# Kernel optimization log

Measured on AMD Instinct MI355X. Metric: run time of the kernel, lower is better.

## Reference

```python
import jax, jax.numpy as jnp
import numpy as np

ZMAX = 92          # max atomic number in NLH table
BOHR = 0.52917721  # Bohr radius in Angstrom (au.BOHR)
ENERGY_UNIT = 1.0  # multiplier for 'Ha'
N_ATOMS = 100_000
N_EDGES = 6_400_000
TAB = (ZMAX + 1) ** 2  # 8649


def setup_inputs() -> dict:
    key = jax.random.key(0)
    k1, k2, k3, k4, k5, k6, k7 = jax.random.split(key, 7)
    species = jax.random.randint(k1, (N_ATOMS,), 0, 93, dtype=jnp.int32)
    edge_src = jax.random.randint(k2, (N_EDGES,), 0, N_ATOMS, dtype=jnp.int32)
    edge_dst = jax.random.randint(k3, (N_EDGES,), 0, N_ATOMS, dtype=jnp.int32)
    # distances kept away from zero (division by rijs)
    distances = 0.5 + 4.5 * jax.random.uniform(k4, (N_EDGES,), dtype=jnp.float32)
    switch = jax.random.uniform(k5, (N_EDGES,), dtype=jnp.float32)
    CS = jax.random.uniform(k6, (TAB, 3), dtype=jnp.float32)
    ALPHAS = jax.random.uniform(k7, (TAB, 3), dtype=jnp.float32) + 0.5
    return {"species": species, "edge_src": edge_src, "edge_dst": edge_dst,
            "distances": distances, "switch": switch, "CS": CS, "ALPHAS": ALPHAS}


def reference(species, edge_src, edge_dst, distances, switch, CS, ALPHAS):
    # pair index into (zmax+1)^2 coefficient table
    s12 = species[edge_src] + ZMAX * species[edge_dst]
    cs = CS[s12]          # [E, 3]
    alphas = ALPHAS[s12]  # [E, 3]
    Z = jnp.where(species > 0, species.astype(distances.dtype), 0.0)
    # 3-term exponential screening function
    phi = jnp.sum(cs * jnp.exp(-alphas * distances[:, None]), axis=-1)  # [E]
    ereppair = Z[edge_src] * Z[edge_dst] * phi * switch / distances
    erep_atomic = ENERGY_UNIT * 0.5 * BOHR * jax.ops.segment_sum(
        ereppair, edge_src, num_segments=species.shape[0])
    return erep_atomic
```

## Files before the change

kernel.cpp:

```cpp
#include <hip/hip_runtime.h>
#include <hip/hip_fp16.h>


#define ZMAX_C 92
#define TAB93  93
#define NTAB   (TAB93 * TAB93)
#define HALF_BOHR 0.264588605f
#define NBMAX 64
#define APB 2048
#define APB_LOG 11
#define SPLITS 16
#define TPB  1024
#define NW   (TPB / 64)
#define TPB2 256
#define EPT 8
#define BLK_EDGES (TPB * EPT)
#define SPC_CAP 122880

typedef int            ivec4 __attribute__((ext_vector_type(4)));
typedef float          fvec4 __attribute__((ext_vector_type(4)));

#if __has_builtin(__builtin_amdgcn_rcpf)
#define FAST_RCP(x) __builtin_amdgcn_rcpf(x)
#else
#define FAST_RCP(x) (1.0f / (x))
#endif

__device__ __forceinline__ float half_lo(unsigned u) {
    return __half2float(*reinterpret_cast<const __half*>(&u));
}
__device__ __forceinline__ float half_hi(unsigned u) {
    unsigned s = u >> 16;
    return __half2float(*reinterpret_cast<const __half*>(&s));
}

__global__ __launch_bounds__(TPB2) void p0_prep(
    const float* __restrict__ CS, const float* __restrict__ ALPHAS,
    const int* __restrict__ species,
    uint4* __restrict__ tab16, unsigned char* __restrict__ spc8,
    unsigned* __restrict__ cursor, float* __restrict__ out,
    int n_atoms, int nb)
{
    int i = blockIdx.x * TPB2 + threadIdx.x;
    if (i < NTAB) {
        int sd = i / TAB93;
        int ss = i - TAB93 * sd;
        int ref = ss + ZMAX_C * sd;
        float Z = (ss > 0 && sd > 0) ? (float)(ss * sd) : 0.0f;
        __half h[8];
        h[0] = __float2half_rn(CS[3*ref+0] * Z);
        h[1] = __float2half_rn(CS[3*ref+1] * Z);
        h[2] = __float2half_rn(CS[3*ref+2] * Z);
        h[3] = __float2half_rn(-ALPHAS[3*ref+0]);
        h[4] = __float2half_rn(-ALPHAS[3*ref+1]);
        h[5] = __float2half_rn(-ALPHAS[3*ref+2]);
        h[6] = __half(0.0f); h[7] = __half(0.0f);
        tab16[i] = *reinterpret_cast<uint4*>(h);
    }
    if (i < n_atoms) {
        spc8[i] = (unsigned char)species[i];
        out[i] = 0.0f;
    }
    if (i < nb) cursor[i] = 0u;
}

__global__ __launch_bounds__(TPB) void p1_bin_lds(
    const int* __restrict__ edge_src, const int* __restrict__ edge_dst,
    const float* __restrict__ dist, const float* __restrict__ swt,
    const unsigned char* __restrict__ spc8, const uint4* __restrict__ tab16,
    unsigned* __restrict__ pairs, unsigned* __restrict__ cursor,
    int nb, int cap, int n_edges, int n_atoms, int nchunks)
{
    __shared__ unsigned char spcL[SPC_CAP];
    __shared__ unsigned stage[BLK_EDGES];
    __shared__ unsigned histW[NW][NBMAX];
    __shared__ unsigned hist[NBMAX];
    __shared__ unsigned lbase[NBMAX];
    __shared__ unsigned gbase[NBMAX];

    int tid = threadIdx.x, bid = blockIdx.x;
    const int G = gridDim.x;
    int lane = tid & 63, wave = tid >> 6;

    {
        uint4* dv = (uint4*)spcL;
        const uint4* sv = (const uint4*)spc8;
        int n16 = (n_atoms + 15) >> 4;
        for (int i = tid; i < n16; i += TPB) dv[i] = sv[i];
    }
    __syncthreads();

    for (int c = bid; c < nchunks; c += G) {
        ((unsigned*)histW)[tid] = 0u;
        __syncthreads();

        long long wbase = (long long)c * BLK_EDGES + (long long)wave * (64 * EPT);
        unsigned meta[EPT];
        unsigned short s12r[EPT];

        {
            int srcv[EPT], dstv[EPT];
            #pragma unroll
            for (int j = 0; j < EPT / 4; ++j) {
                long long e0 = wbase + j * 256 + lane * 4;
                if (e0 + 3 < (long long)n_edges) {
                    ivec4 s4 = *reinterpret_cast<const ivec4*>(edge_src + e0);
                    ivec4 d4 = *reinterpret_cast<const ivec4*>(edge_dst + e0);
                    #pragma unroll
                    for (int k = 0; k < 4; ++k) { srcv[j*4+k] = s4[k]; dstv[j*4+k] = d4[k]; }
                } else {
                    #pragma unroll
                    for (int k = 0; k < 4; ++k) {
                        long long e = e0 + k;
                        bool v = (e < (long long)n_edges);
                        srcv[j*4+k] = v ? edge_src[e] : 0;
                        dstv[j*4+k] = v ? edge_dst[e] : 0;
                    }
                }
            }
            int ssv[EPT], sdv[EPT];
            #pragma unroll
            for (int i = 0; i < EPT; ++i) ssv[i] = spcL[srcv[i]];
            #pragma unroll
            for (int i = 0; i < EPT; ++i) sdv[i] = spcL[dstv[i]];
            #pragma unroll
            for (int j = 0; j < EPT / 4; ++j) {
                long long e0 = wbase + j * 256 + lane * 4;
                #pragma unroll
                for (int k = 0; k < 4; ++k) {
                    int idx = j * 4 + k;
                    s12r[idx] = (unsigned short)(ssv[idx] + TAB93 * sdv[idx]);
                    meta[idx] = 0u;
                    if (e0 + k < (long long)n_edges) {
                        unsigned b    = (unsigned)srcv[idx] >> APB_LOG;
                        unsigned lsrc = (unsigned)srcv[idx] & (APB - 1);
                        unsigned rank = atomicAdd(&histW[wave][b], 1u);
                        meta[idx] = 0x80000000u | (rank << 17) | (b << 11) | lsrc;
                    }
                }
            }
        }
        __syncthreads();
        if (tid < 64) {
            unsigned run = 0;
            #pragma unroll
            for (int w = 0; w < NW; ++w) {
                unsigned t = histW[w][tid];
                histW[w][tid] = run;
                run += t;
            }
            unsigned tot = run;
            if (tid < nb) hist[tid] = tot;
            unsigned v = (tid < nb) ? tot : 0u;
            unsigned x = v;
            #pragma unroll
            for (int off = 1; off < 64; off <<= 1) {
                unsigned y = __shfl_up(x, off);
                if ((tid & 63) >= off) x += y;
            }
            if (tid < nb) {
                lbase[tid] = x - v;
                gbase[tid] = v ? atomicAdd(cursor + tid, v) : 0u;
            }
        }
        __syncthreads();

        {
            long long eA = wbase + lane * 4;
            long long eB = wbase + 256 + lane * 4;
            float rA[4], wA[4], rB[4], wB[4];
            bool fullB = (eB + 3 < (long long)n_edges);
            if (fullB) {
                fvec4 r4 = *reinterpret_cast<const fvec4*>(dist + eA);
                fvec4 w4 = *reinterpret_cast<const fvec4*>(swt + eA);
                fvec4 r5 = *reinterpret_cast<const fvec4*>(dist + eB);
                fvec4 w5 = *reinterpret_cast<const fvec4*>(swt + eB);
                #pragma unroll
                for (int k = 0; k < 4; ++k) {
                    rA[k] = r4[k]; wA[k] = w4[k]; rB[k] = r5[k]; wB[k] = w5[k];
                }
            } else {
                #pragma unroll
                for (int k = 0; k < 4; ++k) {
                    long long ea = eA + k, eb = eB + k;
                    bool va = (ea < (long long)n_edges), vb = (eb < (long long)n_edges);
                    rA[k] = va ? dist[ea] : 1.f;  wA[k] = va ? swt[ea] : 0.f;
                    rB[k] = vb ? dist[eb] : 1.f;  wB[k] = vb ? swt[eb] : 0.f;
                }
            }
            uint4 tA[4], tB[4];
            #pragma unroll
            for (int k = 0; k < 4; ++k) tA[k] = tab16[s12r[k]];
            #pragma unroll
            for (int k = 0; k < 4; ++k) tB[k] = tab16[s12r[4 + k]];
            #pragma unroll
            for (int g = 0; g < 2; ++g) {
                const float* r = g ? rB : rA;
                const float* w = g ? wB : wA;
                const uint4* t = g ? tB : tA;
                #pragma unroll
                for (int k = 0; k < 4; ++k) {
                    int idx = g * 4 + k;
                    unsigned m = meta[idx];
                    if (!(m & 0x80000000u)) continue;
                    float c0 = half_lo(t[k].x), c1 = half_hi(t[k].x);
                    float c2 = half_lo(t[k].y), na0 = half_hi(t[k].y);
                    float na1 = half_lo(t[k].z), na2 = half_hi(t[k].z);
                    float phi = c0 * __expf(na0 * r[k])
                              + c1 * __expf(na1 * r[k])
                              + c2 * __expf(na2 * r[k]);
                    float val = HALF_BOHR * phi * w[k] * FAST_RCP(r[k]);
                    unsigned b = (m >> 11) & 63u;
                    unsigned pos = lbase[b] + histW[wave][b] + ((m >> 17) & 0x3FFFu);
                    unsigned short hb = __half_as_ushort(__float2half_rn(val));
                    stage[pos] = ((m & (APB - 1)) << 16) | (unsigned)hb;
                }
            }
        }
        __syncthreads();
        for (int b = wave; b < nb; b += NW) {
            unsigned cnt = hist[b], lb = lbase[b], gb = gbase[b];
            unsigned* dst = pairs + (size_t)b * (size_t)cap + gb;
            for (unsigned i = lane; i < cnt; i += 64)
                if (gb + i < (unsigned)cap) dst[i] = stage[lb + i];
        }
    }
}

#define TPBF 256
#define NWF  4
#define BLKF (TPBF * EPT)
__global__ __launch_bounds__(TPBF) void p1_bin(
    const int* __restrict__ edge_src, const int* __restrict__ edge_dst,
    const float* __restrict__ dist, const float* __restrict__ swt,
    const unsigned char* __restrict__ spc8, const uint4* __restrict__ tab16,
    unsigned* __restrict__ pairs, unsigned* __restrict__ cursor,
    int nb, int cap, int n_edges)
{
    __shared__ unsigned stage[BLKF];
    __shared__ unsigned hist4[NWF][NBMAX];
    __shared__ unsigned hist[NBMAX];
    __shared__ unsigned lbase[NBMAX];
    __shared__ unsigned gbase[NBMAX];

    int tid = threadIdx.x;
    ((unsigned*)hist4)[tid] = 0u;
    __syncthreads();

    int lane = tid & 63, wave = tid >> 6;
    long long wbase = (long long)blockIdx.x * BLKF + (long long)wave * (64 * EPT);

    unsigned meta[EPT];
    unsigned short s12r[EPT];
    {
        int srcv[EPT], dstv[EPT];
        #pragma unroll
        for (int j = 0; j < EPT / 4; ++j) {
            long long e0 = wbase + j * 256 + lane * 4;
            if (e0 + 3 < (long long)n_edges) {
                ivec4 s4 = *reinterpret_cast<const ivec4*>(edge_src + e0);
                ivec4 d4 = *reinterpret_cast<const ivec4*>(edge_dst + e0);
                #pragma unroll
                for (int k = 0; k < 4; ++k) { srcv[j*4+k] = s4[k]; dstv[j*4+k] = d4[k]; }
            } else {
                #pragma unroll
                for (int k = 0; k < 4; ++k) {
                    long long e = e0 + k;
                    bool v = (e < (long long)n_edges);
                    srcv[j*4+k] = v ? edge_src[e] : 0;
                    dstv[j*4+k] = v ? edge_dst[e] : 0;
                }
            }
        }
        int ssv[EPT], sdv[EPT];
        #pragma unroll
        for (int i = 0; i < EPT; ++i) ssv[i] = spc8[srcv[i]];
        #pragma unroll
        for (int i = 0; i < EPT; ++i) sdv[i] = spc8[dstv[i]];
        #pragma unroll
        for (int j = 0; j < EPT / 4; ++j) {
            long long e0 = wbase + j * 256 + lane * 4;
            #pragma unroll
            for (int k = 0; k < 4; ++k) {
                int idx = j * 4 + k;
                s12r[idx] = (unsigned short)(ssv[idx] + TAB93 * sdv[idx]);
                meta[idx] = 0u;
                if (e0 + k < (long long)n_edges) {
                    unsigned b    = (unsigned)srcv[idx] >> APB_LOG;
                    unsigned lsrc = (unsigned)srcv[idx] & (APB - 1);
                    unsigned rank = atomicAdd(&hist4[wave][b], 1u);
                    meta[idx] = 0x80000000u | (rank << 17) | (b << 11) | lsrc;
                }
            }
        }
    }
    __syncthreads();
    if (tid < 64) {
        unsigned run = 0;
        #pragma unroll
        for (int w = 0; w < NWF; ++w) {
            unsigned t = hist4[w][tid];
            hist4[w][tid] = run;
            run += t;
        }
        unsigned tot = run;
        if (tid < nb) hist[tid] = tot;
        unsigned v = (tid < nb) ? tot : 0u;
        unsigned x = v;
        #pragma unroll
        for (int off = 1; off < 64; off <<= 1) {
            unsigned y = __shfl_up(x, off);
            if ((tid & 63) >= off) x += y;
        }
        if (tid < nb) {
            lbase[tid] = x - v;
            gbase[tid] = v ? atomicAdd(cursor + tid, v) : 0u;
        }
    }
    __syncthreads();
    {
        long long eA = wbase + lane * 4;
        long long eB = wbase + 256 + lane * 4;
        float rA[4], wA[4], rB[4], wB[4];
        bool fullB = (eB + 3 < (long long)n_edges);
        if (fullB) {
            fvec4 r4 = *reinterpret_cast<const fvec4*>(dist + eA);
            fvec4 w4 = *reinterpret_cast<const fvec4*>(swt + eA);
            fvec4 r5 = *reinterpret_cast<const fvec4*>(dist + eB);
            fvec4 w5 = *reinterpret_cast<const fvec4*>(swt + eB);
            #pragma unroll
            for (int k = 0; k < 4; ++k) {
                rA[k] = r4[k]; wA[k] = w4[k]; rB[k] = r5[k]; wB[k] = w5[k];
            }
        } else {
            #pragma unroll
            for (int k = 0; k < 4; ++k) {
                long long ea = eA + k, eb = eB + k;
                bool va = (ea < (long long)n_edges), vb = (eb < (long long)n_edges);
                rA[k] = va ? dist[ea] : 1.f;  wA[k] = va ? swt[ea] : 0.f;
                rB[k] = vb ? dist[eb] : 1.f;  wB[k] = vb ? swt[eb] : 0.f;
            }
        }
        uint4 tA[4], tB[4];
        #pragma unroll
        for (int k = 0; k < 4; ++k) tA[k] = tab16[s12r[k]];
        #pragma unroll
        for (int k = 0; k < 4; ++k) tB[k] = tab16[s12r[4 + k]];
        #pragma unroll
        for (int g = 0; g < 2; ++g) {
            const float* r = g ? rB : rA;
            const float* w = g ? wB : wA;
            const uint4* t = g ? tB : tA;
            #pragma unroll
            for (int k = 0; k < 4; ++k) {
                int idx = g * 4 + k;
                unsigned m = meta[idx];
                if (!(m & 0x80000000u)) continue;
                float c0 = half_lo(t[k].x), c1 = half_hi(t[k].x);
                float c2 = half_lo(t[k].y), na0 = half_hi(t[k].y);
                float na1 = half_lo(t[k].z), na2 = half_hi(t[k].z);
                float phi = c0 * __expf(na0 * r[k])
                          + c1 * __expf(na1 * r[k])
                          + c2 * __expf(na2 * r[k]);
                float val = HALF_BOHR * phi * w[k] * FAST_RCP(r[k]);
                unsigned b = (m >> 11) & 63u;
                unsigned pos = lbase[b] + hist4[wave][b] + ((m >> 17) & 0x3FFFu);
                unsigned short hb = __half_as_ushort(__float2half_rn(val));
                stage[pos] = ((m & (APB - 1)) << 16) | (unsigned)hb;
            }
        }
    }
    __syncthreads();
    for (int b = wave; b < nb; b += NWF) {
        unsigned cnt = hist[b], lb = lbase[b], gb = gbase[b];
        unsigned* dst = pairs + (size_t)b * (size_t)cap + gb;
        for (unsigned i = lane; i < cnt; i += 64)
            if (gb + i < (unsigned)cap) dst[i] = stage[lb + i];
    }
}

__global__ __launch_bounds__(TPB2) void p2a_reduce(
    const unsigned* __restrict__ pairs, const unsigned* __restrict__ cursor,
    float* __restrict__ out, int cap, int n_atoms)
{
    int b = blockIdx.x / SPLITS;
    int s = blockIdx.x % SPLITS;
    __shared__ float acc[APB];
    for (int i = threadIdx.x; i < APB; i += TPB2) acc[i] = 0.f;
    __syncthreads();
    unsigned cnt = cursor[b];
    if (cnt > (unsigned)cap) cnt = (unsigned)cap;
    unsigned nq = (cnt + 3u) >> 2;
    unsigned qb = (unsigned)((unsigned long long)nq * s / SPLITS);
    unsigned qe = (unsigned)((unsigned long long)nq * (s + 1) / SPLITS);
    const uint4* p4 = (const uint4*)(pairs + (size_t)b * (size_t)cap);
    for (unsigned q = qb + threadIdx.x; q < qe; q += TPB2) {
        uint4 v = p4[q];
        unsigned base = q << 2;
        if (base + 3u < cnt) {
            unsafeAtomicAdd(&acc[v.x >> 16], __half2float(__ushort_as_half((unsigned short)(v.x & 0xFFFFu))));
            unsafeAtomicAdd(&acc[v.y >> 16], __half2float(__ushort_as_half((unsigned short)(v.y & 0xFFFFu))));
            unsafeAtomicAdd(&acc[v.z >> 16], __half2float(__ushort_as_half((unsigned short)(v.z & 0xFFFFu))));
            unsafeAtomicAdd(&acc[v.w >> 16], __half2float(__ushort_as_half((unsigned short)(v.w & 0xFFFFu))));
        } else {
            unsigned vv[4] = {v.x, v.y, v.z, v.w};
            #pragma unroll
            for (int e = 0; e < 4; ++e)
                if (base + (unsigned)e < cnt)
                    unsafeAtomicAdd(&acc[vv[e] >> 16],
                        __half2float(__ushort_as_half((unsigned short)(vv[e] & 0xFFFFu))));
        }
    }
    __syncthreads();
    int abase = b * APB;
    for (int k = threadIdx.x; k < APB; k += TPB2) {
        int atom = abase + k;
        float vv = acc[k];
        if (atom < n_atoms && vv != 0.0f)
            unsafeAtomicAdd(&out[atom], vv);
    }
}

__global__ __launch_bounds__(TPB2) void erep_edges_direct(
    const int* __restrict__ edge_src, const int* __restrict__ edge_dst,
    const float* __restrict__ dist, const float* __restrict__ swt,
    const int* __restrict__ species, const float* __restrict__ CS,
    const float* __restrict__ ALPHAS, float* __restrict__ out, int n_edges)
{
    int e = blockIdx.x * TPB2 + threadIdx.x;
    if (e >= n_edges) return;
    int ss = species[edge_src[e]], sd = species[edge_dst[e]];
    int prod = ss * sd;
    if (prod == 0) return;
    int s12 = ss + ZMAX_C * sd;
    float r = dist[e];
    float phi = CS[3*s12+0] * __expf(-ALPHAS[3*s12+0] * r)
              + CS[3*s12+1] * __expf(-ALPHAS[3*s12+1] * r)
              + CS[3*s12+2] * __expf(-ALPHAS[3*s12+2] * r);
    atomicAdd(out + edge_src[e],
              HALF_BOHR * (float)prod * phi * swt[e] * FAST_RCP(r));
}

extern "C" void kernel_launch(void* const* d_in, const int* in_sizes, int n_in,
                              void* d_out, int out_size, void* d_ws, size_t ws_size,
                              hipStream_t stream)
{
    const int*   species  = (const int*)  d_in[0];
    const int*   edge_src = (const int*)  d_in[1];
    const int*   edge_dst = (const int*)  d_in[2];
    const float* dist     = (const float*)d_in[3];
    const float* swt      = (const float*)d_in[4];
    const float* CS       = (const float*)d_in[5];
    const float* ALPHAS   = (const float*)d_in[6];
    float* out = (float*)d_out;

    int n_atoms = in_sizes[0];
    int n_edges = in_sizes[1];

    int nb = (n_atoms + APB - 1) / APB;
    long long capll = (long long)n_edges / nb + (long long)n_edges / ((long long)nb * 32) + 256;
    int cap = (int)((capll + 31) & ~31LL);

    size_t pairs_sz = ((size_t)nb * (size_t)cap * 4 + 255) & ~(size_t)255;
    size_t cur_sz   = ((size_t)nb * 4 + 255) & ~(size_t)255;
    size_t tab_sz   = ((size_t)NTAB * 16 + 255) & ~(size_t)255;
    size_t spc_sz   = ((size_t)n_atoms + 255) & ~(size_t)255;
    size_t need = pairs_sz + cur_sz + tab_sz + spc_sz;

    if (nb <= NBMAX && n_edges > 0 && ws_size >= need) {
        char* w = (char*)d_ws;
        unsigned*       pairs   = (unsigned*)w;
        unsigned*       cursor  = (unsigned*)(w + pairs_sz);
        uint4*          tab16   = (uint4*)(w + pairs_sz + cur_sz);
        unsigned char*  spc8    = (unsigned char*)(w + pairs_sz + cur_sz + tab_sz);

        int pmax = n_atoms > NTAB ? n_atoms : NTAB;
        p0_prep<<<(pmax + TPB2 - 1) / TPB2, TPB2, 0, stream>>>(
            CS, ALPHAS, species, tab16, spc8, cursor, out, n_atoms, nb);

        if (n_atoms <= SPC_CAP) {
            int dev = 0, ncu = 256;
            (void)hipGetDevice(&dev);
            (void)hipDeviceGetAttribute(&ncu, hipDeviceAttributeMultiprocessorCount, dev);
            int nchunks = (int)(((long long)n_edges + BLK_EDGES - 1) / BLK_EDGES);
            int G = ncu > 0 ? ncu : 256;
            if (G > nchunks) G = nchunks;
            p1_bin_lds<<<G, TPB, 0, stream>>>(
                edge_src, edge_dst, dist, swt, spc8, tab16,
                pairs, cursor, nb, cap, n_edges, n_atoms, nchunks);
        } else {
            p1_bin<<<(n_edges + BLKF - 1) / BLKF, TPBF, 0, stream>>>(
                edge_src, edge_dst, dist, swt, spc8, tab16,
                pairs, cursor, nb, cap, n_edges);
        }

        p2a_reduce<<<nb * SPLITS, TPB2, 0, stream>>>(pairs, cursor, out, cap, n_atoms);
    } else {
        (void)hipMemsetAsync(d_out, 0, (size_t)out_size * sizeof(float), stream);
        erep_edges_direct<<<(n_edges + TPB2 - 1) / TPB2, TPB2, 0, stream>>>(
            edge_src, edge_dst, dist, swt, species, CS, ALPHAS, out, n_edges);
    }
}
```

Measured before the change: 233.6 us.

## Replace LDS binning and reduce pass with direct global atomic accumulation

```diff
diff --git a/kernel.cpp b/kernel.cpp
--- a/kernel.cpp
+++ b/kernel.cpp
@@ -11,7 +11,6 @@
 #define APB_LOG 11
 #define SPLITS 16
 #define TPB  1024
-#define NW   (TPB / 64)
 #define TPB2 256
 #define EPT 8
 #define BLK_EDGES (TPB * EPT)
@@ -64,19 +63,13 @@
     if (i < nb) cursor[i] = 0u;
 }
 
-__global__ __launch_bounds__(TPB) void p1_bin_lds(
+__global__ __launch_bounds__(TPB) void p1_direct(
     const int* __restrict__ edge_src, const int* __restrict__ edge_dst,
     const float* __restrict__ dist, const float* __restrict__ swt,
     const unsigned char* __restrict__ spc8, const uint4* __restrict__ tab16,
-    unsigned* __restrict__ pairs, unsigned* __restrict__ cursor,
-    int nb, int cap, int n_edges, int n_atoms, int nchunks)
+    float* __restrict__ out, int n_edges, int n_atoms, int nchunks)
 {
     __shared__ unsigned char spcL[SPC_CAP];
-    __shared__ unsigned stage[BLK_EDGES];
-    __shared__ unsigned histW[NW][NBMAX];
-    __shared__ unsigned hist[NBMAX];
-    __shared__ unsigned lbase[NBMAX];
-    __shared__ unsigned gbase[NBMAX];
 
     int tid = threadIdx.x, bid = blockIdx.x;
     const int G = gridDim.x;
@@ -91,15 +84,13 @@
     __syncthreads();
 
     for (int c = bid; c < nchunks; c += G) {
-        ((unsigned*)histW)[tid] = 0u;
-        __syncthreads();
-
         long long wbase = (long long)c * BLK_EDGES + (long long)wave * (64 * EPT);
-        unsigned meta[EPT];
+
+        int srcv[EPT];
         unsigned short s12r[EPT];
 
         {
-            int srcv[EPT], dstv[EPT];
+            int dstv[EPT];
             #pragma unroll
             for (int j = 0; j < EPT / 4; ++j) {
                 long long e0 = wbase + j * 256 + lane * 4;
@@ -124,46 +115,9 @@
             #pragma unroll
             for (int i = 0; i < EPT; ++i) sdv[i] = spcL[dstv[i]];
             #pragma unroll
-            for (int j = 0; j < EPT / 4; ++j) {
-                long long e0 = wbase + j * 256 + lane * 4;
-                #pragma unroll
-                for (int k = 0; k < 4; ++k) {
-                    int idx = j * 4 + k;
-                    s12r[idx] = (unsigned short)(ssv[idx] + TAB93 * sdv[idx]);
-                    meta[idx] = 0u;
-                    if (e0 + k < (long long)n_edges) {
-                        unsigned b    = (unsigned)srcv[idx] >> APB_LOG;
-                        unsigned lsrc = (unsigned)srcv[idx] & (APB - 1);
-                        unsigned rank = atomicAdd(&histW[wave][b], 1u);
-                        meta[idx] = 0x80000000u | (rank << 17) | (b << 11) | lsrc;
-                    }
-                }
-            }
-        }
-        __syncthreads();
-        if (tid < 64) {
-            unsigned run = 0;
-            #pragma unroll
-            for (int w = 0; w < NW; ++w) {
-                unsigned t = histW[w][tid];
-                histW[w][tid] = run;
-                run += t;
-            }
-            unsigned tot = run;
-            if (tid < nb) hist[tid] = tot;
-            unsigned v = (tid < nb) ? tot : 0u;
-            unsigned x = v;
-            #pragma unroll
-            for (int off = 1; off < 64; off <<= 1) {
-                unsigned y = __shfl_up(x, off);
-                if ((tid & 63) >= off) x += y;
-            }
-            if (tid < nb) {
-                lbase[tid] = x - v;
-                gbase[tid] = v ? atomicAdd(cursor + tid, v) : 0u;
-            }
-        }
-        __syncthreads();
+            for (int i = 0; i < EPT; ++i)
+                s12r[i] = (unsigned short)(ssv[i] + TAB93 * sdv[i]);
+        }
 
         {
             long long eA = wbase + lane * 4;
@@ -201,8 +155,6 @@
                 #pragma unroll
                 for (int k = 0; k < 4; ++k) {
                     int idx = g * 4 + k;
-                    unsigned m = meta[idx];
-                    if (!(m & 0x80000000u)) continue;
                     float c0 = half_lo(t[k].x), c1 = half_hi(t[k].x);
                     float c2 = half_lo(t[k].y), na0 = half_hi(t[k].y);
                     float na1 = half_lo(t[k].z), na2 = half_hi(t[k].z);
@@ -210,19 +162,10 @@
                               + c1 * __expf(na1 * r[k])
                               + c2 * __expf(na2 * r[k]);
                     float val = HALF_BOHR * phi * w[k] * FAST_RCP(r[k]);
-                    unsigned b = (m >> 11) & 63u;
-                    unsigned pos = lbase[b] + histW[wave][b] + ((m >> 17) & 0x3FFFu);
-                    unsigned short hb = __half_as_ushort(__float2half_rn(val));
-                    stage[pos] = ((m & (APB - 1)) << 16) | (unsigned)hb;
-                }
-            }
-        }
-        __syncthreads();
-        for (int b = wave; b < nb; b += NW) {
-            unsigned cnt = hist[b], lb = lbase[b], gb = gbase[b];
-            unsigned* dst = pairs + (size_t)b * (size_t)cap + gb;
-            for (unsigned i = lane; i < cnt; i += 64)
-                if (gb + i < (unsigned)cap) dst[i] = stage[lb + i];
+                    if (val != 0.0f)
+                        unsafeAtomicAdd(&out[srcv[idx]], val);
+                }
+            }
         }
     }
 }
@@ -485,16 +428,15 @@
             int nchunks = (int)(((long long)n_edges + BLK_EDGES - 1) / BLK_EDGES);
             int G = ncu > 0 ? ncu : 256;
             if (G > nchunks) G = nchunks;
-            p1_bin_lds<<<G, TPB, 0, stream>>>(
+            p1_direct<<<G, TPB, 0, stream>>>(
                 edge_src, edge_dst, dist, swt, spc8, tab16,
-                pairs, cursor, nb, cap, n_edges, n_atoms, nchunks);
+                out, n_edges, n_atoms, nchunks);
         } else {
             p1_bin<<<(n_edges + BLKF - 1) / BLKF, TPBF, 0, stream>>>(
                 edge_src, edge_dst, dist, swt, spc8, tab16,
                 pairs, cursor, nb, cap, n_edges);
-        }
-
-        p2a_reduce<<<nb * SPLITS, TPB2, 0, stream>>>(pairs, cursor, out, cap, n_atoms);
+            p2a_reduce<<<nb * SPLITS, TPB2, 0, stream>>>(pairs, cursor, out, cap, n_atoms);
+        }
     } else {
         (void)hipMemsetAsync(d_out, 0, (size_t)out_size * sizeof(float), stream);
         erep_edges_direct<<<(n_edges + TPB2 - 1) / TPB2, TPB2, 0, stream>>>(
```

New measurement: 456.9 us. 95.6% more time.
